# Kernel optimization log

Hardware: AMD Instinct MI355X
Metric: run time of the kernel (lower is better)

Reference implementation:

```python
import jax, jax.numpy as jnp
import numpy as np
import math

B, N, C, S, H, E = 2, 20000, 512, 128, 8, 320000
D = C // H
EPS = 1e-6


def setup_inputs() -> dict:
    key = jax.random.key(0)
    ks = jax.random.split(key, 14)
    x = jax.random.normal(ks[0], (B, N, C), jnp.float32)
    adj_indices = jax.random.randint(ks[1], (2, E), 0, N)
    adj_values = jax.random.uniform(ks[2], (E,), jnp.float32)

    def lin(k, fi, fo):
        # stored as (in, out) so y = x @ W + b (equivalent to torch Linear)
        return jax.random.normal(k, (fi, fo), jnp.float32) / np.sqrt(fi).astype(np.float32)

    Ws = lin(ks[3], C, S); bs = jnp.zeros((S,), jnp.float32)
    Wq = lin(ks[4], C, C); bq = jnp.zeros((C,), jnp.float32)
    Wk = lin(ks[5], C, C); bk = jnp.zeros((C,), jnp.float32)
    Wv = lin(ks[6], C, C); bv = jnp.zeros((C,), jnp.float32)
    Wo = lin(ks[7], C, C); bo = jnp.zeros((C,), jnp.float32)
    beta_raw = jnp.float32(math.log(math.expm1(0.13)))
    return {"x": x, "adj_indices": adj_indices, "adj_values": adj_values,
            "Ws": Ws, "bs": bs, "Wq": Wq, "bq": bq, "Wk": Wk, "bk": bk,
            "Wv": Wv, "bv": bv, "Wo": Wo, "bo": bo, "beta_raw": beta_raw}


def reference(x, adj_indices, adj_values, Ws, bs, Wq, bq, Wk, bk, Wv, bv, Wo, bo, beta_raw):
    # slice assignment weights: (B, N, S)
    weights = jax.nn.softmax(x @ Ws + bs, axis=-1)
    # weight_sum -> (B, S, 1), clamped
    wsum = jnp.maximum(weights.sum(axis=1), EPS)[:, :, None]
    slices = jnp.einsum('bns,bnc->bsc', weights, x) / wsum  # (B, S, C)

    # sparse adjacency aggregation: y[b, r] = sum_e v_e * weights[b, col_e]
    rows, cols = adj_indices[0], adj_indices[1]
    msg = jnp.take(weights, cols, axis=1) * adj_values[None, :, None]  # (B, E, S)
    graph_weights = jax.vmap(lambda m: jax.ops.segment_sum(m, rows, num_segments=N))(msg)  # (B, N, S)

    gb = jnp.einsum('bns,bnt->bst', weights, graph_weights)  # (B, S, S)
    gb = 0.5 * (gb + jnp.swapaxes(gb, 1, 2))
    gb = gb / jnp.maximum(gb.sum(axis=-1, keepdims=True), EPS)
    gb = jnp.log(jnp.maximum(gb, EPS))

    def heads(t, W, b):
        return (t @ W + b).reshape(B, S, H, D).transpose(0, 2, 1, 3)  # (B, H, S, D)

    q = heads(slices, Wq, bq)
    k = heads(slices, Wk, bk)
    v = heads(slices, Wv, bv)
    logits = jnp.einsum('bhqd,bhkd->bhqk', q, k) / math.sqrt(D)
    logits = logits + jax.nn.softplus(beta_raw) * gb[:, None]
    attn = jax.nn.softmax(logits, axis=-1)
    slices_out = jnp.einsum('bhqk,bhkd->bhqd', attn, v).transpose(0, 2, 1, 3).reshape(B, S, C)
    slices_out = slices_out @ Wo + bo
    return jnp.einsum('bns,bsc->bnc', weights, slices_out)  # (B, N, C)
```

## Files before the change

### kernel.cpp

```cpp
#include <hip/hip_runtime.h>
#include <math.h>

#define Bn 2
#define Nn 20000
#define Cn 512
#define Sn 128
#define Hn 8
#define Dn 64
#define En 320000
#define EPSf 1e-6f
#define NB64 313
#define NB128 157

#define S_CHUNK 320
#define S_KB 63
#define G_CHUNK 128
#define G_KB 157

typedef __attribute__((ext_vector_type(4))) float f32x4;
typedef __attribute__((ext_vector_type(8))) short s16x8;

__device__ __forceinline__ unsigned short f2bf(float f) {
    unsigned u = __float_as_uint(f);
    return (unsigned short)((u + 0x7fffu + ((u >> 16) & 1u)) >> 16);
}
__device__ __forceinline__ float bf2f(unsigned short h) {
    return __uint_as_float(((unsigned)h) << 16);
}

__device__ __forceinline__ unsigned lds_off(int row, int n) {
    unsigned ch = ((((unsigned)n >> 3) ^ ((unsigned)row & 7u) ^ (((unsigned)row >> 3) & 7u)) & 7u);
    return (unsigned)row * 128u + ch * 16u + ((unsigned)n & 7u) * 2u;
}

__device__ __forceinline__ void stage_bf16tile(
    const unsigned short* __restrict__ src, int stride, int nvalid, unsigned* dst, int t)
{
    #pragma unroll
    for (int l = 0; l < 2; l++) {
        int task = t + l * 256;
        int row = task >> 2, seg = task & 3;
        s16x8 a = {0,0,0,0,0,0,0,0}, b = {0,0,0,0,0,0,0,0};
        if (row < nvalid) {
            a = *(const s16x8*)(src + (size_t)row * stride + seg * 16);
            b = *(const s16x8*)(src + (size_t)row * stride + seg * 16 + 8);
        }
        *(s16x8*)((char*)dst + lds_off(row, seg * 16)) = a;
        *(s16x8*)((char*)dst + lds_off(row, seg * 16 + 8)) = b;
    }
}

__device__ __forceinline__ void stage_pairtile(
    const unsigned short* __restrict__ src, int stride, int c0,
    int nbase, int nlimit, unsigned* dst, int t)
{
    int c = t & 15;
    int p0 = t >> 4;
    #pragma unroll
    for (int half = 0; half < 2; half++) {
        int pp = p0 + half * 16;
        int nl = 2 * pp;
        int ng = nbase + nl;
        s16x8 a0 = {0,0,0,0,0,0,0,0}, a1 = {0,0,0,0,0,0,0,0};
        if (ng < nlimit)     a0 = *(const s16x8*)(src + (size_t)ng * stride + c0 + 8 * c);
        if (ng + 1 < nlimit) a1 = *(const s16x8*)(src + (size_t)(ng + 1) * stride + c0 + 8 * c);
        #pragma unroll
        for (int i = 0; i < 8; i++) {
            unsigned val = ((unsigned)(unsigned short)a0[i]) |
                           (((unsigned)(unsigned short)a1[i]) << 16);
            dst[lds_off(8 * c + i, nl) >> 2] = val;
        }
    }
}

__global__ __launch_bounds__(256) void k_prepW(
    const float* __restrict__ Ws, const float* __restrict__ Wq,
    const float* __restrict__ Wk, const float* __restrict__ Wv,
    const float* __restrict__ Wo, unsigned short* __restrict__ WsT,
    unsigned short* __restrict__ WT, int* __restrict__ zeroU,
    float* __restrict__ wsum)
{
    __shared__ float tile[32][33];
    int t = threadIdx.x;
    int z = blockIdx.z;
    int k0 = blockIdx.x * 32;
    int c0 = blockIdx.y * 32;
    const float* W;
    unsigned short* dst;
    int ncols;
    if (z == 0) {
        if (c0 >= Sn) {
            int idx = (((int)blockIdx.y - 4) * 16 + (int)blockIdx.x) * 256 + t;
            if (idx < 40064) zeroU[idx] = 0;
            else if (idx < 40064 + Bn * Sn) wsum[idx - 40064] = 0.f;
            return;
        }
        W = Ws; dst = WsT; ncols = Sn;
    } else {
        W = (z == 1) ? Wq : (z == 2) ? Wk : (z == 3) ? Wv : Wo;
        dst = WT + (size_t)(z - 1) * Cn * Cn; ncols = Cn;
    }
    #pragma unroll
    for (int l = 0; l < 4; l++) {
        int idx = t + l * 256;
        int r = idx >> 5, c = idx & 31;
        tile[r][c] = W[(size_t)(k0 + r) * ncols + c0 + c];
    }
    __syncthreads();
    #pragma unroll
    for (int l = 0; l < 4; l++) {
        int idx = t + l * 256;
        int r = idx >> 5, c = idx & 31;
        dst[(size_t)(c0 + r) * Cn + k0 + c] = f2bf(tile[c][r]);
    }
}

__global__ __launch_bounds__(256) void k_assign2(
    const float* __restrict__ x, const unsigned short* __restrict__ WsT,
    const float* __restrict__ bs, unsigned short* __restrict__ weights,
    float* __restrict__ wsum)
{
    __shared__ __align__(16) unsigned At32[2][2048];
    __shared__ __align__(16) unsigned Bt32[2][4096];
    __shared__ float wsum_loc[128];

    int t = threadIdx.x;
    int lane = t & 63;
    int wid = t >> 6;
    int l15 = lane & 15, lg = lane >> 4;
    int blk = blockIdx.x;
    int b = blk / NB64;
    int rb = blk % NB64;
    int n0 = rb * 64;
    int nvalid = Nn - n0; if (nvalid > 64) nvalid = 64;
    const float* xb = x + (size_t)b * Nn * Cn;

    if (t < 128) wsum_loc[t] = 0.f;

    int arow = t >> 2, aseg = t & 3;
    bool aok = (arow < nvalid);
    const float4* aptr = (const float4*)(xb + (size_t)(n0 + arow) * Cn) + aseg * 4;
    int brow = t >> 2, bseg = t & 3;
    const unsigned short* bp0 = WsT + (size_t)brow * Cn + bseg * 16;
    const unsigned short* bp1 = WsT + (size_t)(brow + 64) * Cn + bseg * 16;

    const f32x4 fz = {0.f, 0.f, 0.f, 0.f};
    f32x4 acc[8];
    #pragma unroll
    for (int j = 0; j < 8; j++) acc[j] = fz;

    float4 ra[4];
    #pragma unroll
    for (int i = 0; i < 4; i++) ra[i] = make_float4(0.f, 0.f, 0.f, 0.f);
    s16x8 rb0a, rb0b, rb1a, rb1b;

    if (aok) { ra[0] = aptr[0]; ra[1] = aptr[1]; ra[2] = aptr[2]; ra[3] = aptr[3]; }
    rb0a = *(const s16x8*)(bp0);     rb0b = *(const s16x8*)(bp0 + 8);
    rb1a = *(const s16x8*)(bp1);     rb1b = *(const s16x8*)(bp1 + 8);

    int cur = 0;
    for (int ks = 0; ks < 8; ks++) {
        {
            float v[16] = {ra[0].x, ra[0].y, ra[0].z, ra[0].w,
                           ra[1].x, ra[1].y, ra[1].z, ra[1].w,
                           ra[2].x, ra[2].y, ra[2].z, ra[2].w,
                           ra[3].x, ra[3].y, ra[3].z, ra[3].w};
            #pragma unroll
            for (int h = 0; h < 2; h++) {
                uint4 u;
                u.x = (unsigned)f2bf(v[h*8+0]) | (((unsigned)f2bf(v[h*8+1])) << 16);
                u.y = (unsigned)f2bf(v[h*8+2]) | (((unsigned)f2bf(v[h*8+3])) << 16);
                u.z = (unsigned)f2bf(v[h*8+4]) | (((unsigned)f2bf(v[h*8+5])) << 16);
                u.w = (unsigned)f2bf(v[h*8+6]) | (((unsigned)f2bf(v[h*8+7])) << 16);
                *(uint4*)((char*)At32[cur] + lds_off(arow, aseg * 16 + h * 8)) = u;
            }
            *(s16x8*)((char*)Bt32[cur] + lds_off(brow, bseg * 16)) = rb0a;
            *(s16x8*)((char*)Bt32[cur] + lds_off(brow, bseg * 16 + 8)) = rb0b;
            *(s16x8*)((char*)Bt32[cur] + lds_off(brow + 64, bseg * 16)) = rb1a;
            *(s16x8*)((char*)Bt32[cur] + lds_off(brow + 64, bseg * 16 + 8)) = rb1b;
        }
        if (ks < 7) {
            int kn = ks + 1;
            if (aok) {
                ra[0] = aptr[kn*16]; ra[1] = aptr[kn*16+1];
                ra[2] = aptr[kn*16+2]; ra[3] = aptr[kn*16+3];
            }
            rb0a = *(const s16x8*)(bp0 + kn*64); rb0b = *(const s16x8*)(bp0 + kn*64 + 8);
            rb1a = *(const s16x8*)(bp1 + kn*64); rb1b = *(const s16x8*)(bp1 + kn*64 + 8);
        }
        __syncthreads();
        #pragma unroll
        for (int m = 0; m < 2; m++) {
            s16x8 af = *(const s16x8*)((const char*)At32[cur] +
                       lds_off(wid * 16 + l15, m * 32 + lg * 8));
            #pragma unroll
            for (int j = 0; j < 8; j++) {
                s16x8 bf = *(const s16x8*)((const char*)Bt32[cur] +
                           lds_off(j * 16 + l15, m * 32 + lg * 8));
                acc[j] = __builtin_amdgcn_mfma_f32_16x16x32_bf16(af, bf, acc[j], 0, 0, 0);
            }
        }
        __syncthreads();
        cur ^= 1;
    }

    float bsv[8];
    #pragma unroll
    for (int j = 0; j < 8; j++) bsv[j] = bs[j * 16 + l15];

    unsigned short* wb = weights + (size_t)b * Nn * Sn;
    unsigned short* wt = (unsigned short*)&At32[0][0];
    float wacc[8] = {0.f,0.f,0.f,0.f,0.f,0.f,0.f,0.f};
    #pragma unroll
    for (int r = 0; r < 4; r++) {
        float lv[8];
        #pragma unroll
        for (int j = 0; j < 8; j++) lv[j] = acc[j][r] + bsv[j];
        float m = lv[0];
        #pragma unroll
        for (int j = 1; j < 8; j++) m = fmaxf(m, lv[j]);
        m = fmaxf(m, __shfl_xor(m, 1));
        m = fmaxf(m, __shfl_xor(m, 2));
        m = fmaxf(m, __shfl_xor(m, 4));
        m = fmaxf(m, __shfl_xor(m, 8));
        float e[8], sm = 0.f;
        #pragma unroll
        for (int j = 0; j < 8; j++) { e[j] = __expf(lv[j] - m); sm += e[j]; }
        sm += __shfl_xor(sm, 1);
        sm += __shfl_xor(sm, 2);
        sm += __shfl_xor(sm, 4);
        sm += __shfl_xor(sm, 8);
        float inv = 1.f / sm;
        int rloc = wid * 16 + lg * 4 + r;
        bool valid = (n0 + rloc < Nn);
        #pragma unroll
        for (int j = 0; j < 8; j++) {
            float w = e[j] * inv;
            wt[rloc * 128 + j * 16 + l15] = f2bf(w);
            if (valid) wacc[j] += w;
        }
    }
    #pragma unroll
    for (int j = 0; j < 8; j++) {
        wacc[j] += __shfl_xor(wacc[j], 16);
        wacc[j] += __shfl_xor(wacc[j], 32);
    }
    if (lg == 0) {
        #pragma unroll
        for (int j = 0; j < 8; j++) atomicAdd(&wsum_loc[j * 16 + l15], wacc[j]);
    }
    __syncthreads();
    {
        int orow = t >> 2, oseg = t & 3;
        if (orow < nvalid) {
            uint4* dst = (uint4*)(wb + (size_t)(n0 + orow) * Sn + oseg * 32);
            const uint4* src = (const uint4*)(wt + (size_t)orow * 128 + oseg * 32);
            dst[0] = src[0]; dst[1] = src[1]; dst[2] = src[2]; dst[3] = src[3];
        }
    }
    if (t < 128) atomicAdd(&wsum[b * Sn + t], wsum_loc[t]);
}

__global__ __launch_bounds__(256) void k_deg(
    const int* __restrict__ adj, int* __restrict__ deg)
{
    int e = blockIdx.x * 256 + threadIdx.x;
    if (e < En) atomicAdd(&deg[adj[e]], 1);
}

__global__ __launch_bounds__(1024) void k_scan(
    const int* __restrict__ deg, int* __restrict__ offs)
{
    __shared__ int wsums[16];
    __shared__ int excl[16];
    __shared__ int runsS;
    __shared__ int totS;
    int t = threadIdx.x;
    int lane = t & 63;
    int w = t >> 6;
    if (t == 0) { offs[0] = 0; runsS = 0; }
    __syncthreads();
    for (int base = 0; base < Nn; base += 1024) {
        int v = (base + t < Nn) ? deg[base + t] : 0;
        int sv = v;
        #pragma unroll
        for (int d = 1; d < 64; d <<= 1) {
            int u = __shfl_up(sv, d);
            if (lane >= d) sv += u;
        }
        if (lane == 63) wsums[w] = sv;
        __syncthreads();
        if (t < 16) {
            int xv = wsums[t];
            int sw = xv;
            #pragma unroll
            for (int d = 1; d < 16; d <<= 1) {
                int u = __shfl_up(sw, d);
                if (t >= d) sw += u;
            }
            excl[t] = sw - xv;
            if (t == 15) totS = sw;
        }
        __syncthreads();
        if (base + t < Nn) offs[base + t + 1] = runsS + excl[w] + sv;
        __syncthreads();
        if (t == 0) runsS += totS;
        __syncthreads();
    }
}

__global__ __launch_bounds__(256) void k_fill(
    const int* __restrict__ adj, const float* __restrict__ vals,
    const int* __restrict__ offs, int* __restrict__ cursor,
    int2* __restrict__ epack)
{
    int e = blockIdx.x * 256 + threadIdx.x;
    if (e < En) {
        int r = adj[e];
        int p = atomicAdd(&cursor[r], 1);
        epack[offs[r] + p] = make_int2(adj[En + e], __float_as_int(vals[e]));
    }
}

__global__ __launch_bounds__(128) void k_gather(
    const unsigned short* __restrict__ weights, const int2* __restrict__ epack,
    const int* __restrict__ offs, unsigned short* __restrict__ gwb)
{
    int r = blockIdx.x;
    int s = threadIdx.x;
    int o0 = offs[r], o1 = offs[r + 1];
    const unsigned short* w0 = weights;
    const unsigned short* w1 = weights + (size_t)Nn * Sn;
    float a0 = 0.f, a1 = 0.f;
    int j = o0;
    for (; j + 4 <= o1; j += 4) {
        int2 e0 = epack[j], e1 = epack[j + 1], e2 = epack[j + 2], e3 = epack[j + 3];
        float v0 = __int_as_float(e0.y), v1 = __int_as_float(e1.y);
        float v2 = __int_as_float(e2.y), v3 = __int_as_float(e3.y);
        float p00 = bf2f(w0[(size_t)e0.x * Sn + s]);
        float p01 = bf2f(w1[(size_t)e0.x * Sn + s]);
        float p10 = bf2f(w0[(size_t)e1.x * Sn + s]);
        float p11 = bf2f(w1[(size_t)e1.x * Sn + s]);
        float p20 = bf2f(w0[(size_t)e2.x * Sn + s]);
        float p21 = bf2f(w1[(size_t)e2.x * Sn + s]);
        float p30 = bf2f(w0[(size_t)e3.x * Sn + s]);
        float p31 = bf2f(w1[(size_t)e3.x * Sn + s]);
        a0 += v0 * p00 + v1 * p10 + v2 * p20 + v3 * p30;
        a1 += v0 * p01 + v1 * p11 + v2 * p21 + v3 * p31;
    }
    for (; j < o1; j++) {
        int2 e = epack[j];
        float v = __int_as_float(e.y);
        a0 += v * bf2f(w0[(size_t)e.x * Sn + s]);
        a1 += v * bf2f(w1[(size_t)e.x * Sn + s]);
    }
    gwb[(size_t)r * Sn + s] = f2bf(a0);
    gwb[(size_t)Nn * Sn + (size_t)r * Sn + s] = f2bf(a1);
}

__global__ __launch_bounds__(256) void k_mmS(
    const unsigned short* __restrict__ wAall, const float* __restrict__ xall,
    float* __restrict__ partial)
{
    __shared__ __align__(16) unsigned At32[2][4096];
    __shared__ __align__(16) unsigned Bt32[2][4096];
    int t = threadIdx.x;
    int lane = t & 63;
    int wid = t >> 6;
    int ws = wid & 1, wc = wid >> 1;
    int blk = blockIdx.x;
    int b = blk / (4 * S_KB);
    int rem = blk % (4 * S_KB);
    int cb = rem / S_KB;
    int kb = rem % S_KB;
    int n0 = kb * S_CHUNK;
    int c0 = cb * 128;
    const unsigned short* wA = wAall + (size_t)b * Nn * Sn;
    const float* Bsrc = xall + (size_t)b * Nn * Cn;

    f32x4 acc[4][4];
    const f32x4 fz = {0.f, 0.f, 0.f, 0.f};
    #pragma unroll
    for (int i = 0; i < 4; i++) {
        #pragma unroll
        for (int j = 0; j < 4; j++) acc[i][j] = fz;
    }

    int l15 = lane & 15, lg = lane >> 4;
    int c = t & 15;
    int p0 = t >> 4;

    s16x8 pa[2][2];
    float4 pb[2][4];
    const s16x8 z8 = {0,0,0,0,0,0,0,0};

    auto LOADS = [&](int kt) {
        #pragma unroll
        for (int h = 0; h < 2; h++) {
            int nl = 2 * (p0 + h * 16);
            int ng = n0 + kt + nl;
            pa[h][0] = z8; pa[h][1] = z8;
            pb[h][0] = make_float4(0.f,0.f,0.f,0.f); pb[h][1] = pb[h][0];
            pb[h][2] = pb[h][0]; pb[h][3] = pb[h][0];
            if (ng < Nn) {
                pa[h][0] = *(const s16x8*)(wA + (size_t)ng * Sn + 8 * c);
                pb[h][0] = *(const float4*)(Bsrc + (size_t)ng * Cn + c0 + 8 * c);
                pb[h][1] = *(const float4*)(Bsrc + (size_t)ng * Cn + c0 + 8 * c + 4);
            }
            if (ng + 1 < Nn) {
                pa[h][1] = *(const s16x8*)(wA + (size_t)(ng + 1) * Sn + 8 * c);
                pb[h][2] = *(const float4*)(Bsrc + (size_t)(ng + 1) * Cn + c0 + 8 * c);
                pb[h][3] = *(const float4*)(Bsrc + (size_t)(ng + 1) * Cn + c0 + 8 * c + 4);
            }
        }
    };
    auto STORE = [&](int buf) {
        #pragma unroll
        for (int h = 0; h < 2; h++) {
            int nl = 2 * (p0 + h * 16);
            #pragma unroll
            for (int i = 0; i < 8; i++) {
                unsigned val = ((unsigned)(unsigned short)pa[h][0][i]) |
                               (((unsigned)(unsigned short)pa[h][1][i]) << 16);
                At32[buf][lds_off(8 * c + i, nl) >> 2] = val;
            }
            float b0[8] = {pb[h][0].x, pb[h][0].y, pb[h][0].z, pb[h][0].w,
                           pb[h][1].x, pb[h][1].y, pb[h][1].z, pb[h][1].w};
            float b1[8] = {pb[h][2].x, pb[h][2].y, pb[h][2].z, pb[h][2].w,
                           pb[h][3].x, pb[h][3].y, pb[h][3].z, pb[h][3].w};
            #pragma unroll
            for (int i = 0; i < 8; i++) {
                unsigned val = (unsigned)f2bf(b0[i]) | (((unsigned)f2bf(b1[i])) << 16);
                Bt32[buf][lds_off(8 * c + i, nl) >> 2] = val;
            }
        }
    };

    LOADS(0);
    int cur = 0;
    for (int it = 0; it < 5; it++) {
        STORE(cur);
        if (it < 4) LOADS((it + 1) * 64);
        __syncthreads();
        #pragma unroll
        for (int m = 0; m < 2; m++) {
            s16x8 af[4], bfr[4];
            #pragma unroll
            for (int i = 0; i < 4; i++) {
                int row = ws * 64 + i * 16 + l15;
                af[i] = *(const s16x8*)((const char*)At32[cur] + lds_off(row, m * 32 + lg * 8));
            }
            #pragma unroll
            for (int j = 0; j < 4; j++) {
                int row = wc * 64 + j * 16 + l15;
                bfr[j] = *(const s16x8*)((const char*)Bt32[cur] + lds_off(row, m * 32 + lg * 8));
            }
            #pragma unroll
            for (int i = 0; i < 4; i++) {
                #pragma unroll
                for (int j = 0; j < 4; j++)
                    acc[i][j] = __builtin_amdgcn_mfma_f32_16x16x32_bf16(
                        af[i], bfr[j], acc[i][j], 0, 0, 0);
            }
        }
        __syncthreads();
        cur ^= 1;
    }

    float* pp = partial + (size_t)blk * 16384;
    #pragma unroll
    for (int i = 0; i < 4; i++) {
        int srow = ws * 64 + i * 16 + lg * 4;
        #pragma unroll
        for (int j = 0; j < 4; j++) {
            int ccol = wc * 64 + j * 16 + l15;
            #pragma unroll
            for (int r = 0; r < 4; r++)
                pp[(size_t)(srow + r) * 128 + ccol] = acc[i][j][r];
        }
    }
}

__global__ __launch_bounds__(256) void k_mmG(
    const unsigned short* __restrict__ wAall, const unsigned short* __restrict__ gwall,
    float* __restrict__ partial)
{
    __shared__ __align__(16) unsigned At32[4096];
    __shared__ __align__(16) unsigned Bt32[4096];
    int t = threadIdx.x;
    int lane = t & 63;
    int wid = t >> 6;
    int ws = wid & 1, wc = wid >> 1;
    int blk = blockIdx.x;
    int b = blk / G_KB;
    int kb = blk % G_KB;
    int n0 = kb * G_CHUNK;
    const unsigned short* wA = wAall + (size_t)b * Nn * Sn;
    const unsigned short* Bsrc = gwall + (size_t)b * Nn * Sn;

    f32x4 acc[4][4];
    const f32x4 fz = {0.f, 0.f, 0.f, 0.f};
    #pragma unroll
    for (int i = 0; i < 4; i++) {
        #pragma unroll
        for (int j = 0; j < 4; j++) acc[i][j] = fz;
    }

    int l15 = lane & 15, lg = lane >> 4;

    for (int kt = 0; kt < G_CHUNK; kt += 64) {
        stage_pairtile(wA, Sn, 0, n0 + kt, Nn, At32, t);
        stage_pairtile(Bsrc, Sn, 0, n0 + kt, Nn, Bt32, t);
        __syncthreads();
        #pragma unroll
        for (int m = 0; m < 2; m++) {
            s16x8 af[4], bfr[4];
            #pragma unroll
            for (int i = 0; i < 4; i++) {
                int row = ws * 64 + i * 16 + l15;
                af[i] = *(const s16x8*)((const char*)At32 + lds_off(row, m * 32 + lg * 8));
            }
            #pragma unroll
            for (int j = 0; j < 4; j++) {
                int row = wc * 64 + j * 16 + l15;
                bfr[j] = *(const s16x8*)((const char*)Bt32 + lds_off(row, m * 32 + lg * 8));
            }
            #pragma unroll
            for (int i = 0; i < 4; i++) {
                #pragma unroll
                for (int j = 0; j < 4; j++)
                    acc[i][j] = __builtin_amdgcn_mfma_f32_16x16x32_bf16(
                        af[i], bfr[j], acc[i][j], 0, 0, 0);
            }
        }
        __syncthreads();
    }

    float* pp = partial + (size_t)blk * 16384;
    #pragma unroll
    for (int i = 0; i < 4; i++) {
        int srow = ws * 64 + i * 16 + lg * 4;
        #pragma unroll
        for (int j = 0; j < 4; j++) {
            int ccol = wc * 64 + j * 16 + l15;
            #pragma unroll
            for (int r = 0; r < 4; r++)
                pp[(size_t)(srow + r) * 128 + ccol] = acc[i][j][r];
        }
    }
}

__global__ __launch_bounds__(256) void k_reduceS(
    const float* __restrict__ partial, const float* __restrict__ wsum,
    unsigned short* __restrict__ sl16)
{
    int g = blockIdx.x * 256 + threadIdx.x;
    int c = g & 127;
    int s = (g >> 7) & 127;
    int cb = (g >> 14) & 3;
    int b = g >> 16;
    const float* pp = partial + (size_t)(b * 4 + cb) * S_KB * 16384 + (size_t)s * 128 + c;
    float sum = 0.f;
    #pragma unroll 7
    for (int kb = 0; kb < S_KB; kb++) sum += pp[(size_t)kb * 16384];
    sl16[((size_t)b * Sn + s) * Cn + cb * 128 + c] =
        f2bf(sum / fmaxf(wsum[b * Sn + s], EPSf));
}

__global__ __launch_bounds__(256) void k_reduceG(
    const float* __restrict__ partial, float* __restrict__ gb_raw)
{
    int g = blockIdx.x * 256 + threadIdx.x;
    int t2 = g & 127;
    int s = (g >> 7) & 127;
    int b = g >> 14;
    const float* pp = partial + (size_t)b * G_KB * 16384 + (size_t)s * 128 + t2;
    float sum = 0.f;
    #pragma unroll 8
    for (int kb = 0; kb < G_KB; kb++) sum += pp[(size_t)kb * 16384];
    gb_raw[(size_t)b * 16384 + (size_t)s * 128 + t2] = sum;
}

__global__ __launch_bounds__(128) void k_gb_fin(
    const float* __restrict__ gb_raw, float* __restrict__ gb)
{
    int bid = blockIdx.x;
    int b = bid >> 7, i = bid & 127;
    int j = threadIdx.x;
    const float* gr = gb_raw + (size_t)b * Sn * Sn;
    float sym = 0.5f * (gr[i * Sn + j] + gr[j * Sn + i]);
    float sum = sym;
    #pragma unroll
    for (int d = 1; d < 64; d <<= 1) sum += __shfl_xor(sum, d);
    __shared__ float wred[2];
    if ((j & 63) == 0) wred[j >> 6] = sum;
    __syncthreads();
    sum = wred[0] + wred[1];
    float r = fmaxf(sum, EPSf);
    gb[(size_t)b * Sn * Sn + (size_t)i * Sn + j] = logf(fmaxf(sym / r, EPSf));
}

__global__ __launch_bounds__(256) void k_qkv(
    const unsigned short* __restrict__ sl16, const unsigned short* __restrict__ WT,
    const float* __restrict__ bq, const float* __restrict__ bk,
    const float* __restrict__ bv,
    float* __restrict__ q, float* __restrict__ kb, float* __restrict__ vb)
{
    __shared__ __align__(16) unsigned At32[4096];
    __shared__ __align__(16) unsigned Bt32[4096];
    int t = threadIdx.x;
    int lane = t & 63;
    int wid = t >> 6;
    int ws = wid & 1, wc = wid >> 1;
    int l15 = lane & 15, lg = lane >> 4;
    int rb = blockIdx.x, cb = blockIdx.y, sel = blockIdx.z;
    const unsigned short* Bmat = WT + (size_t)sel * Cn * Cn;
    const float* bias = (sel == 0) ? bq : (sel == 1) ? bk : bv;
    float* outp = (sel == 0) ? q : (sel == 1) ? kb : vb;

    f32x4 acc[4][4];
    const f32x4 fz = {0.f, 0.f, 0.f, 0.f};
    #pragma unroll
    for (int i = 0; i < 4; i++) {
        #pragma unroll
        for (int j = 0; j < 4; j++) acc[i][j] = fz;
    }

    for (int ks = 0; ks < 8; ks++) {
        stage_bf16tile(sl16 + (size_t)rb * 128 * Cn + ks * 64, Cn, 128, At32, t);
        stage_bf16tile(Bmat + (size_t)cb * 128 * Cn + ks * 64, Cn, 128, Bt32, t);
        __syncthreads();
        #pragma unroll
        for (int m = 0; m < 2; m++) {
            s16x8 af[4], bfr[4];
            #pragma unroll
            for (int i = 0; i < 4; i++)
                af[i] = *(const s16x8*)((const char*)At32 +
                        lds_off(ws * 64 + i * 16 + l15, m * 32 + lg * 8));
            #pragma unroll
            for (int j = 0; j < 4; j++)
                bfr[j] = *(const s16x8*)((const char*)Bt32 +
                        lds_off(wc * 64 + j * 16 + l15, m * 32 + lg * 8));
            #pragma unroll
            for (int i = 0; i < 4; i++) {
                #pragma unroll
                for (int j = 0; j < 4; j++)
                    acc[i][j] = __builtin_amdgcn_mfma_f32_16x16x32_bf16(
                        af[i], bfr[j], acc[i][j], 0, 0, 0);
            }
        }
        __syncthreads();
    }

    float bvv[4];
    #pragma unroll
    for (int j = 0; j < 4; j++) bvv[j] = bias[cb * 128 + wc * 64 + j * 16 + l15];
    #pragma unroll
    for (int i = 0; i < 4; i++) {
        #pragma unroll
        for (int r = 0; r < 4; r++) {
            int m = rb * 128 + ws * 64 + i * 16 + lg * 4 + r;
            #pragma unroll
            for (int j = 0; j < 4; j++)
                outp[(size_t)m * Cn + cb * 128 + wc * 64 + j * 16 + l15] =
                    acc[i][j][r] + bvv[j];
        }
    }
}

__global__ __launch_bounds__(128) void k_attn(
    const float* __restrict__ q, const float* __restrict__ k,
    const float* __restrict__ v, const float* __restrict__ gb,
    const float* __restrict__ beta_raw, unsigned short* __restrict__ attn16)
{
    __shared__ float kv[128][65];
    __shared__ float qv[64];
    __shared__ float p[128];
    __shared__ float wred[2][2];

    int t = threadIdx.x;
    int bid = blockIdx.x;
    int b = bid / (Hn * Sn);
    int h = (bid / Sn) % Hn;
    int i = bid % Sn;
    size_t base = (size_t)b * Sn * Cn + (size_t)h * Dn;

    if (t < 64) qv[t] = q[base + (size_t)i * Cn + t];
    for (int l = 0; l < 64; l++) {
        int idx = t + l * 128;
        int j = idx >> 6, d = idx & 63;
        kv[j][d] = k[base + (size_t)j * Cn + d];
    }
    __syncthreads();

    float dot = 0.f;
    #pragma unroll
    for (int d = 0; d < 64; d++) dot += qv[d] * kv[t][d];

    float beta = log1pf(__expf(beta_raw[0]));
    float logit = dot * 0.125f + beta * gb[(size_t)b * Sn * Sn + (size_t)i * Sn + t];

    float m = logit;
    #pragma unroll
    for (int d = 1; d < 64; d <<= 1) m = fmaxf(m, __shfl_xor(m, d));
    if ((t & 63) == 0) wred[0][t >> 6] = m;
    __syncthreads();
    m = fmaxf(wred[0][0], wred[0][1]);
    float e = __expf(logit - m);
    float sm = e;
    #pragma unroll
    for (int d = 1; d < 64; d <<= 1) sm += __shfl_xor(sm, d);
    if ((t & 63) == 0) wred[1][t >> 6] = sm;
    __syncthreads();
    sm = wred[1][0] + wred[1][1];
    p[t] = e / sm;
    __syncthreads();

    for (int l = 0; l < 64; l++) {
        int idx = t + l * 128;
        int j = idx >> 6, d = idx & 63;
        kv[j][d] = v[base + (size_t)j * Cn + d];
    }
    __syncthreads();

    if (t < 64) {
        float o = 0.f;
        #pragma unroll 8
        for (int j = 0; j < 128; j++) o += p[j] * kv[j][t];
        attn16[base + (size_t)i * Cn + t] = f2bf(o);
    }
}

__global__ __launch_bounds__(256) void k_wo(
    const unsigned short* __restrict__ attn16, const unsigned short* __restrict__ WoT,
    const float* __restrict__ bo, unsigned short* __restrict__ SoT)
{
    __shared__ __align__(16) unsigned At32[4096];
    __shared__ __align__(16) unsigned Bt32[4096];
    int t = threadIdx.x;
    int lane = t & 63;
    int wid = t >> 6;
    int ws = wid & 1, wc = wid >> 1;
    int l15 = lane & 15, lg = lane >> 4;
    int b = blockIdx.x, cb = blockIdx.y;

    f32x4 acc[4][4];
    const f32x4 fz = {0.f, 0.f, 0.f, 0.f};
    #pragma unroll
    for (int i = 0; i < 4; i++) {
        #pragma unroll
        for (int j = 0; j < 4; j++) acc[i][j] = fz;
    }

    for (int ks = 0; ks < 8; ks++) {
        stage_bf16tile(attn16 + (size_t)b * 128 * Cn + ks * 64, Cn, 128, At32, t);
        stage_bf16tile(WoT + (size_t)cb * 128 * Cn + ks * 64, Cn, 128, Bt32, t);
        __syncthreads();
        #pragma unroll
        for (int m = 0; m < 2; m++) {
            s16x8 af[4], bfr[4];
            #pragma unroll
            for (int i = 0; i < 4; i++)
                af[i] = *(const s16x8*)((const char*)At32 +
                        lds_off(ws * 64 + i * 16 + l15, m * 32 + lg * 8));
            #pragma unroll
            for (int j = 0; j < 4; j++)
                bfr[j] = *(const s16x8*)((const char*)Bt32 +
                        lds_off(wc * 64 + j * 16 + l15, m * 32 + lg * 8));
            #pragma unroll
            for (int i = 0; i < 4; i++) {
                #pragma unroll
                for (int j = 0; j < 4; j++)
                    acc[i][j] = __builtin_amdgcn_mfma_f32_16x16x32_bf16(
                        af[i], bfr[j], acc[i][j], 0, 0, 0);
            }
        }
        __syncthreads();
    }

    float bvv[4];
    #pragma unroll
    for (int j = 0; j < 4; j++) bvv[j] = bo[cb * 128 + wc * 64 + j * 16 + l15];
    unsigned short* sb = SoT + (size_t)b * Cn * Sn;
    #pragma unroll
    for (int i = 0; i < 4; i++) {
        #pragma unroll
        for (int j = 0; j < 4; j++) {
            int c = cb * 128 + wc * 64 + j * 16 + l15;
            #pragma unroll
            for (int r = 0; r < 4; r++) {
                int s = ws * 64 + i * 16 + lg * 4 + r;
                sb[(size_t)c * Sn + s] = f2bf(acc[i][j][r] + bvv[j]);
            }
        }
    }
}

__global__ __launch_bounds__(256) void k_out2(
    const unsigned short* __restrict__ wAll, const unsigned short* __restrict__ SoT,
    float* __restrict__ out)
{
    __shared__ __align__(16) unsigned At32[4096];
    __shared__ __align__(16) unsigned Bt32[4096];
    int t = threadIdx.x;
    int lane = t & 63;
    int wid = t >> 6;
    int ws = wid & 1, wc = wid >> 1;
    int l15 = lane & 15, lg = lane >> 4;
    int blk = blockIdx.x;
    int b = blk / (NB128 * 4);
    int rem = blk % (NB128 * 4);
    int rb = rem >> 2;
    int cb = rem & 3;
    int n0 = rb * 128, c0 = cb * 128;
    int nvalid = Nn - n0; if (nvalid > 128) nvalid = 128;
    const unsigned short* wb = wAll + (size_t)b * Nn * Sn;
    const unsigned short* sb = SoT + (size_t)b * Cn * Sn;

    f32x4 acc[4][4];
    const f32x4 fz = {0.f, 0.f, 0.f, 0.f};
    #pragma unroll
    for (int i = 0; i < 4; i++) {
        #pragma unroll
        for (int j = 0; j < 4; j++) acc[i][j] = fz;
    }

    #pragma unroll
    for (int ksi = 0; ksi < 2; ksi++) {
        stage_bf16tile(wb + (size_t)n0 * Sn + ksi * 64, Sn, nvalid, At32, t);
        stage_bf16tile(sb + (size_t)c0 * Sn + ksi * 64, Sn, 128, Bt32, t);
        __syncthreads();
        #pragma unroll
        for (int m = 0; m < 2; m++) {
            s16x8 af[4], bfr[4];
            #pragma unroll
            for (int i = 0; i < 4; i++)
                af[i] = *(const s16x8*)((const char*)At32 +
                        lds_off(ws * 64 + i * 16 + l15, m * 32 + lg * 8));
            #pragma unroll
            for (int j = 0; j < 4; j++)
                bfr[j] = *(const s16x8*)((const char*)Bt32 +
                        lds_off(wc * 64 + j * 16 + l15, m * 32 + lg * 8));
            #pragma unroll
            for (int i = 0; i < 4; i++) {
                #pragma unroll
                for (int j = 0; j < 4; j++)
                    acc[i][j] = __builtin_amdgcn_mfma_f32_16x16x32_bf16(
                        af[i], bfr[j], acc[i][j], 0, 0, 0);
            }
        }
        __syncthreads();
    }

    #pragma unroll
    for (int i = 0; i < 4; i++) {
        #pragma unroll
        for (int r = 0; r < 4; r++) {
            int n = n0 + ws * 64 + i * 16 + lg * 4 + r;
            if (n < Nn) {
                #pragma unroll
                for (int j = 0; j < 4; j++)
                    out[((size_t)b * Nn + n) * Cn + c0 + wc * 64 + j * 16 + l15] =
                        acc[i][j][r];
            }
        }
    }
}

extern "C" void kernel_launch(void* const* d_in, const int* in_sizes, int n_in,
                              void* d_out, int out_size, void* d_ws, size_t ws_size,
                              hipStream_t stream)
{
    const float* x  = (const float*)d_in[0];
    const int* adj  = (const int*)d_in[1];
    const float* av = (const float*)d_in[2];
    const float* Ws = (const float*)d_in[3];
    const float* bs = (const float*)d_in[4];
    const float* Wq = (const float*)d_in[5];
    const float* bq = (const float*)d_in[6];
    const float* Wk = (const float*)d_in[7];
    const float* bk = (const float*)d_in[8];
    const float* Wv = (const float*)d_in[9];
    const float* bv = (const float*)d_in[10];
    const float* Wo = (const float*)d_in[11];
    const float* bo = (const float*)d_in[12];
    const float* br = (const float*)d_in[13];
    float* out = (float*)d_out;
    (void)in_sizes; (void)n_in; (void)out_size; (void)ws_size;

    char* ws = (char*)d_ws;
    size_t off = 0;
    unsigned short* wb16  = (unsigned short*)(ws + off); off += (size_t)Bn * Nn * Sn * 2;
    unsigned short* gwb16 = (unsigned short*)(ws + off); off += (size_t)Bn * Nn * Sn * 2;
    unsigned short* sl16  = (unsigned short*)(ws + off); off += (size_t)Bn * Sn * Cn * 2;
    float* wsum       = (float*)(ws + off); off += 1024;
    float* gb_raw     = (float*)(ws + off); off += (size_t)Bn * Sn * Sn * 4;
    float* gb         = (float*)(ws + off); off += (size_t)Bn * Sn * Sn * 4;
    float* q          = (float*)(ws + off); off += (size_t)Bn * Sn * Cn * 4;
    float* kbuf       = (float*)(ws + off); off += (size_t)Bn * Sn * Cn * 4;
    float* vbuf       = (float*)(ws + off); off += (size_t)Bn * Sn * Cn * 4;
    unsigned short* attn16 = (unsigned short*)(ws + off); off += (size_t)Bn * Sn * Cn * 2;
    unsigned short* WsT = (unsigned short*)(ws + off); off += (size_t)Sn * Cn * 2;
    unsigned short* WT  = (unsigned short*)(ws + off); off += (size_t)4 * Cn * Cn * 2;
    unsigned short* SoT = (unsigned short*)(ws + off); off += (size_t)Bn * Cn * Sn * 2;
    char* U = ws + off;
    int*  deg    = (int*)(U);
    int*  cursor = (int*)(U + 80128);
    int*  offs   = (int*)(U + 160256);
    int2* epack  = (int2*)(U + 240640);
    float* partialS = (float*)U;
    float* partialG = (float*)U;

    k_prepW<<<dim3(16, 16, 5), 256, 0, stream>>>(Ws, Wq, Wk, Wv, Wo, WsT, WT,
                                                 (int*)U, wsum);
    k_assign2<<<Bn * NB64, 256, 0, stream>>>(x, WsT, bs, wb16, wsum);

    k_deg<<<(En + 255) / 256, 256, 0, stream>>>(adj, deg);
    k_scan<<<1, 1024, 0, stream>>>(deg, offs);
    k_fill<<<(En + 255) / 256, 256, 0, stream>>>(adj, av, offs, cursor, epack);
    k_gather<<<Nn, 128, 0, stream>>>(wb16, epack, offs, gwb16);

    k_mmS<<<Bn * 4 * S_KB, 256, 0, stream>>>(wb16, x, partialS);
    k_reduceS<<<(Bn * Sn * Cn) / 256, 256, 0, stream>>>(partialS, wsum, sl16);

    k_mmG<<<Bn * G_KB, 256, 0, stream>>>(wb16, gwb16, partialG);
    k_reduceG<<<(Bn * Sn * Sn) / 256, 256, 0, stream>>>(partialG, gb_raw);
    k_gb_fin<<<Bn * Sn, 128, 0, stream>>>(gb_raw, gb);

    k_qkv<<<dim3(2, 4, 3), 256, 0, stream>>>(sl16, WT, bq, bk, bv, q, kbuf, vbuf);
    k_attn<<<Bn * Hn * Sn, 128, 0, stream>>>(q, kbuf, vbuf, gb, br, attn16);
    k_wo<<<dim3(2, 4), 256, 0, stream>>>(attn16, WT + (size_t)3 * Cn * Cn, bo, SoT);

    k_out2<<<Bn * NB128 * 4, 256, 0, stream>>>(wb16, SoT, out);
}
```

Before: 248.4 us.

## Parallelize degree scan, vectorize gather, double-buffer mmG, merge reductions

```diff
diff --git a/kernel.cpp b/kernel.cpp
--- a/kernel.cpp
+++ b/kernel.cpp
@@ -11,6 +11,7 @@
 #define EPSf 1e-6f
 #define NB64 313
 #define NB128 157
+#define NSCAN 20
 
 #define S_CHUNK 320
 #define S_KB 63
@@ -47,29 +48,6 @@
         }
         *(s16x8*)((char*)dst + lds_off(row, seg * 16)) = a;
         *(s16x8*)((char*)dst + lds_off(row, seg * 16 + 8)) = b;
-    }
-}
-
-__device__ __forceinline__ void stage_pairtile(
-    const unsigned short* __restrict__ src, int stride, int c0,
-    int nbase, int nlimit, unsigned* dst, int t)
-{
-    int c = t & 15;
-    int p0 = t >> 4;
-    #pragma unroll
-    for (int half = 0; half < 2; half++) {
-        int pp = p0 + half * 16;
-        int nl = 2 * pp;
-        int ng = nbase + nl;
-        s16x8 a0 = {0,0,0,0,0,0,0,0}, a1 = {0,0,0,0,0,0,0,0};
-        if (ng < nlimit)     a0 = *(const s16x8*)(src + (size_t)ng * stride + c0 + 8 * c);
-        if (ng + 1 < nlimit) a1 = *(const s16x8*)(src + (size_t)(ng + 1) * stride + c0 + 8 * c);
-        #pragma unroll
-        for (int i = 0; i < 8; i++) {
-            unsigned val = ((unsigned)(unsigned short)a0[i]) |
-                           (((unsigned)(unsigned short)a1[i]) << 16);
-            dst[lds_off(8 * c + i, nl) >> 2] = val;
-        }
     }
 }
 
@@ -268,45 +246,54 @@
     if (e < En) atomicAdd(&deg[adj[e]], 1);
 }
 
-__global__ __launch_bounds__(1024) void k_scan(
-    const int* __restrict__ deg, int* __restrict__ offs)
+__global__ __launch_bounds__(1024) void k_scanA(
+    const int* __restrict__ deg, int* __restrict__ offs, int* __restrict__ bsum)
 {
     __shared__ int wsums[16];
     __shared__ int excl[16];
-    __shared__ int runsS;
-    __shared__ int totS;
     int t = threadIdx.x;
     int lane = t & 63;
     int w = t >> 6;
-    if (t == 0) { offs[0] = 0; runsS = 0; }
-    __syncthreads();
-    for (int base = 0; base < Nn; base += 1024) {
-        int v = (base + t < Nn) ? deg[base + t] : 0;
-        int sv = v;
-        #pragma unroll
-        for (int d = 1; d < 64; d <<= 1) {
-            int u = __shfl_up(sv, d);
-            if (lane >= d) sv += u;
-        }
-        if (lane == 63) wsums[w] = sv;
-        __syncthreads();
-        if (t < 16) {
-            int xv = wsums[t];
-            int sw = xv;
-            #pragma unroll
-            for (int d = 1; d < 16; d <<= 1) {
-                int u = __shfl_up(sw, d);
-                if (t >= d) sw += u;
-            }
-            excl[t] = sw - xv;
-            if (t == 15) totS = sw;
-        }
-        __syncthreads();
-        if (base + t < Nn) offs[base + t + 1] = runsS + excl[w] + sv;
-        __syncthreads();
-        if (t == 0) runsS += totS;
-        __syncthreads();
-    }
+    int base = blockIdx.x * 1024;
+    int v = (base + t < Nn) ? deg[base + t] : 0;
+    int sv = v;
+    #pragma unroll
+    for (int d = 1; d < 64; d <<= 1) {
+        int u = __shfl_up(sv, d);
+        if (lane >= d) sv += u;
+    }
+    if (lane == 63) wsums[w] = sv;
+    __syncthreads();
+    if (t < 16) {
+        int xv = wsums[t];
+        int sw = xv;
+        #pragma unroll
+        for (int d = 1; d < 16; d <<= 1) {
+            int u = __shfl_up(sw, d);
+            if (t >= d) sw += u;
+        }
+        excl[t] = sw - xv;
+        if (t == 15) bsum[blockIdx.x] = sw;
+    }
+    __syncthreads();
+    if (base + t < Nn) offs[base + t + 1] = excl[w] + sv;
+    if (blockIdx.x == 0 && t == 0) offs[0] = 0;
+}
+
+__global__ __launch_bounds__(1024) void k_scanB(
+    int* __restrict__ offs, const int* __restrict__ bsum)
+{
+    __shared__ int pS;
+    int t = threadIdx.x;
+    int blk = blockIdx.x;
+    if (t == 0) {
+        int p = 0;
+        for (int j = 0; j < blk; j++) p += bsum[j];
+        pS = p;
+    }
+    __syncthreads();
+    int base = blk * 1024;
+    if (blk > 0 && base + t < Nn) offs[base + t + 1] += pS;
 }
 
 __global__ __launch_bounds__(256) void k_fill(
@@ -326,36 +313,39 @@
     const unsigned short* __restrict__ weights, const int2* __restrict__ epack,
     const int* __restrict__ offs, unsigned short* __restrict__ gwb)
 {
+    __shared__ float red[2][8][132];
     int r = blockIdx.x;
-    int s = threadIdx.x;
+    int t = threadIdx.x;
+    int eg = t >> 4;
+    int sc = t & 15;
     int o0 = offs[r], o1 = offs[r + 1];
     const unsigned short* w0 = weights;
     const unsigned short* w1 = weights + (size_t)Nn * Sn;
-    float a0 = 0.f, a1 = 0.f;
-    int j = o0;
-    for (; j + 4 <= o1; j += 4) {
-        int2 e0 = epack[j], e1 = epack[j + 1], e2 = epack[j + 2], e3 = epack[j + 3];
-        float v0 = __int_as_float(e0.y), v1 = __int_as_float(e1.y);
-        float v2 = __int_as_float(e2.y), v3 = __int_as_float(e3.y);
-        float p00 = bf2f(w0[(size_t)e0.x * Sn + s]);
-        float p01 = bf2f(w1[(size_t)e0.x * Sn + s]);
-        float p10 = bf2f(w0[(size_t)e1.x * Sn + s]);
-        float p11 = bf2f(w1[(size_t)e1.x * Sn + s]);
-        float p20 = bf2f(w0[(size_t)e2.x * Sn + s]);
-        float p21 = bf2f(w1[(size_t)e2.x * Sn + s]);
-        float p30 = bf2f(w0[(size_t)e3.x * Sn + s]);
-        float p31 = bf2f(w1[(size_t)e3.x * Sn + s]);
-        a0 += v0 * p00 + v1 * p10 + v2 * p20 + v3 * p30;
-        a1 += v0 * p01 + v1 * p11 + v2 * p21 + v3 * p31;
-    }
-    for (; j < o1; j++) {
+    float a0[8], a1[8];
+    #pragma unroll
+    for (int i = 0; i < 8; i++) { a0[i] = 0.f; a1[i] = 0.f; }
+    for (int j = o0 + eg; j < o1; j += 8) {
         int2 e = epack[j];
         float v = __int_as_float(e.y);
-        a0 += v * bf2f(w0[(size_t)e.x * Sn + s]);
-        a1 += v * bf2f(w1[(size_t)e.x * Sn + s]);
-    }
-    gwb[(size_t)r * Sn + s] = f2bf(a0);
-    gwb[(size_t)Nn * Sn + (size_t)r * Sn + s] = f2bf(a1);
+        s16x8 x0 = *(const s16x8*)(w0 + (size_t)e.x * Sn + sc * 8);
+        s16x8 x1 = *(const s16x8*)(w1 + (size_t)e.x * Sn + sc * 8);
+        #pragma unroll
+        for (int i = 0; i < 8; i++) {
+            a0[i] += v * bf2f((unsigned short)x0[i]);
+            a1[i] += v * bf2f((unsigned short)x1[i]);
+        }
+    }
+    #pragma unroll
+    for (int i = 0; i < 8; i++) {
+        red[0][eg][sc * 8 + i] = a0[i];
+        red[1][eg][sc * 8 + i] = a1[i];
+    }
+    __syncthreads();
+    float s0 = 0.f, s1 = 0.f;
+    #pragma unroll
+    for (int gix = 0; gix < 8; gix++) { s0 += red[0][gix][t]; s1 += red[1][gix][t]; }
+    gwb[(size_t)r * Sn + t] = f2bf(s0);
+    gwb[(size_t)Nn * Sn + (size_t)r * Sn + t] = f2bf(s1);
 }
 
 __global__ __launch_bounds__(256) void k_mmS(
@@ -485,8 +475,8 @@
     const unsigned short* __restrict__ wAall, const unsigned short* __restrict__ gwall,
     float* __restrict__ partial)
 {
-    __shared__ __align__(16) unsigned At32[4096];
-    __shared__ __align__(16) unsigned Bt32[4096];
+    __shared__ __align__(16) unsigned At32[2][4096];
+    __shared__ __align__(16) unsigned Bt32[2][4096];
     int t = threadIdx.x;
     int lane = t & 63;
     int wid = t >> 6;
@@ -507,10 +497,49 @@
     }
 
     int l15 = lane & 15, lg = lane >> 4;
-
-    for (int kt = 0; kt < G_CHUNK; kt += 64) {
-        stage_pairtile(wA, Sn, 0, n0 + kt, Nn, At32, t);
-        stage_pairtile(Bsrc, Sn, 0, n0 + kt, Nn, Bt32, t);
+    int c = t & 15;
+    int p0 = t >> 4;
+
+    s16x8 pa[2][2], pg[2][2];
+    const s16x8 z8 = {0,0,0,0,0,0,0,0};
+
+    auto LOADS = [&](int kt) {
+        #pragma unroll
+        for (int h = 0; h < 2; h++) {
+            int nl = 2 * (p0 + h * 16);
+            int ng = n0 + kt + nl;
+            pa[h][0] = z8; pa[h][1] = z8; pg[h][0] = z8; pg[h][1] = z8;
+            if (ng < Nn) {
+                pa[h][0] = *(const s16x8*)(wA + (size_t)ng * Sn + 8 * c);
+                pg[h][0] = *(const s16x8*)(Bsrc + (size_t)ng * Sn + 8 * c);
+            }
+            if (ng + 1 < Nn) {
+                pa[h][1] = *(const s16x8*)(wA + (size_t)(ng + 1) * Sn + 8 * c);
+                pg[h][1] = *(const s16x8*)(Bsrc + (size_t)(ng + 1) * Sn + 8 * c);
+            }
+        }
+    };
+    auto STORE = [&](int buf) {
+        #pragma unroll
+        for (int h = 0; h < 2; h++) {
+            int nl = 2 * (p0 + h * 16);
+            #pragma unroll
+            for (int i = 0; i < 8; i++) {
+                unsigned va = ((unsigned)(unsigned short)pa[h][0][i]) |
+                              (((unsigned)(unsigned short)pa[h][1][i]) << 16);
+                At32[buf][lds_off(8 * c + i, nl) >> 2] = va;
+                unsigned vg = ((unsigned)(unsigned short)pg[h][0][i]) |
+                              (((unsigned)(unsigned short)pg[h][1][i]) << 16);
+                Bt32[buf][lds_off(8 * c + i, nl) >> 2] = vg;
+            }
+        }
+    };
+
+    LOADS(0);
+    int cur = 0;
+    for (int it = 0; it < 2; it++) {
+        STORE(cur);
+        if (it < 1) LOADS(64);
         __syncthreads();
         #pragma unroll
         for (int m = 0; m < 2; m++) {
@@ -518,12 +547,12 @@
             #pragma unroll
             for (int i = 0; i < 4; i++) {
                 int row = ws * 64 + i * 16 + l15;
-                af[i] = *(const s16x8*)((const char*)At32 + lds_off(row, m * 32 + lg * 8));
+                af[i] = *(const s16x8*)((const char*)At32[cur] + lds_off(row, m * 32 + lg * 8));
             }
             #pragma unroll
             for (int j = 0; j < 4; j++) {
                 int row = wc * 64 + j * 16 + l15;
-                bfr[j] = *(const s16x8*)((const char*)Bt32 + lds_off(row, m * 32 + lg * 8));
+                bfr[j] = *(const s16x8*)((const char*)Bt32[cur] + lds_off(row, m * 32 + lg * 8));
             }
             #pragma unroll
             for (int i = 0; i < 4; i++) {
@@ -534,6 +563,7 @@
             }
         }
         __syncthreads();
+        cur ^= 1;
     }
 
     float* pp = partial + (size_t)blk * 16384;
@@ -550,35 +580,34 @@
     }
 }
 
-__global__ __launch_bounds__(256) void k_reduceS(
-    const float* __restrict__ partial, const float* __restrict__ wsum,
-    unsigned short* __restrict__ sl16)
+__global__ __launch_bounds__(256) void k_reduceSG(
+    const float* __restrict__ pS, const float* __restrict__ pG,
+    const float* __restrict__ wsum, unsigned short* __restrict__ sl16,
+    float* __restrict__ gb_raw)
 {
     int g = blockIdx.x * 256 + threadIdx.x;
-    int c = g & 127;
-    int s = (g >> 7) & 127;
-    int cb = (g >> 14) & 3;
-    int b = g >> 16;
-    const float* pp = partial + (size_t)(b * 4 + cb) * S_KB * 16384 + (size_t)s * 128 + c;
-    float sum = 0.f;
-    #pragma unroll 7
-    for (int kb = 0; kb < S_KB; kb++) sum += pp[(size_t)kb * 16384];
-    sl16[((size_t)b * Sn + s) * Cn + cb * 128 + c] =
-        f2bf(sum / fmaxf(wsum[b * Sn + s], EPSf));
-}
-
-__global__ __launch_bounds__(256) void k_reduceG(
-    const float* __restrict__ partial, float* __restrict__ gb_raw)
-{
-    int g = blockIdx.x * 256 + threadIdx.x;
-    int t2 = g & 127;
-    int s = (g >> 7) & 127;
-    int b = g >> 14;
-    const float* pp = partial + (size_t)b * G_KB * 16384 + (size_t)s * 128 + t2;
-    float sum = 0.f;
-    #pragma unroll 8
-    for (int kb = 0; kb < G_KB; kb++) sum += pp[(size_t)kb * 16384];
-    gb_raw[(size_t)b * 16384 + (size_t)s * 128 + t2] = sum;
+    if (g < Bn * Sn * Cn) {
+        int c = g & 127;
+        int s = (g >> 7) & 127;
+        int cb = (g >> 14) & 3;
+        int b = g >> 16;
+        const float* pp = pS + (size_t)(b * 4 + cb) * S_KB * 16384 + (size_t)s * 128 + c;
+        float sum = 0.f;
+        #pragma unroll 7
+        for (int kb = 0; kb < S_KB; kb++) sum += pp[(size_t)kb * 16384];
+        sl16[((size_t)b * Sn + s) * Cn + cb * 128 + c] =
+            f2bf(sum / fmaxf(wsum[b * Sn + s], EPSf));
+    } else {
+        int g2 = g - Bn * Sn * Cn;
+        int t2 = g2 & 127;
+        int s = (g2 >> 7) & 127;
+        int b = g2 >> 14;
+        const float* pp = pG + (size_t)b * G_KB * 16384 + (size_t)s * 128 + t2;
+        float sum = 0.f;
+        #pragma unroll 8
+        for (int kb = 0; kb < G_KB; kb++) sum += pp[(size_t)kb * 16384];
+        gb_raw[(size_t)b * 16384 + (size_t)s * 128 + t2] = sum;
+    }
 }
 
 __global__ __launch_bounds__(128) void k_gb_fin(
@@ -908,23 +937,24 @@
     int*  cursor = (int*)(U + 80128);
     int*  offs   = (int*)(U + 160256);
     int2* epack  = (int2*)(U + 240640);
+    int*  bsum   = (int*)(U + 2800640);
     float* partialS = (float*)U;
-    float* partialG = (float*)U;
+    float* partialG = (float*)(U + (size_t)504 * 65536);
 
     k_prepW<<<dim3(16, 16, 5), 256, 0, stream>>>(Ws, Wq, Wk, Wv, Wo, WsT, WT,
                                                  (int*)U, wsum);
     k_assign2<<<Bn * NB64, 256, 0, stream>>>(x, WsT, bs, wb16, wsum);
 
     k_deg<<<(En + 255) / 256, 256, 0, stream>>>(adj, deg);
-    k_scan<<<1, 1024, 0, stream>>>(deg, offs);
+    k_scanA<<<NSCAN, 1024, 0, stream>>>(deg, offs, bsum);
+    k_scanB<<<NSCAN, 1024, 0, stream>>>(offs, bsum);
     k_fill<<<(En + 255) / 256, 256, 0, stream>>>(adj, av, offs, cursor, epack);
     k_gather<<<Nn, 128, 0, stream>>>(wb16, epack, offs, gwb16);
 
     k_mmS<<<Bn * 4 * S_KB, 256, 0, stream>>>(wb16, x, partialS);
-    k_reduceS<<<(Bn * Sn * Cn) / 256, 256, 0, stream>>>(partialS, wsum, sl16);
-
     k_mmG<<<Bn * G_KB, 256, 0, stream>>>(wb16, gwb16, partialG);
-    k_reduceG<<<(Bn * Sn * Sn) / 256, 256, 0, stream>>>(partialG, gb_raw);
+    k_reduceSG<<<(Bn * Sn * Cn + Bn * Sn * Sn) / 256, 256, 0, stream>>>(
+        partialS, partialG, wsum, sl16, gb_raw);
     k_gb_fin<<<Bn * Sn, 128, 0, stream>>>(gb_raw, gb);
 
     k_qkv<<<dim3(2, 4, 3), 256, 0, stream>>>(sl16, WT, bq, bk, bv, q, kbuf, vbuf);
```

New measurement: 228.6 us. -8.0%, faster.
